# Optimization experiments

Measured on AMD Instinct MI355X. Metric: run time of the kernel, lower is better.

Reference implementation:

```python
import jax, jax.numpy as jnp
import numpy as np

EPS = 1e-6

def _l2norm(t):
    # F.normalize over channel axis (axis=1) of (B, dk, L)
    n = jnp.sqrt(jnp.sum(t * t, axis=1, keepdims=True))
    return t / jnp.maximum(n, EPS)

def setup_inputs() -> dict:
    key = jax.random.key(0)
    ks = jax.random.split(key, 8)
    B, Cin, Cenc, dk, dv, H, W = 2, 64, 96, 64, 64, 96, 96
    return {
        "x": jax.random.normal(ks[0], (B, Cin, H, W), dtype=jnp.float32),
        "x_enc": jax.random.normal(ks[1], (B, Cenc, H, W), dtype=jnp.float32),
        "Wq": jax.random.normal(ks[2], (dk, Cenc), dtype=jnp.float32) * 0.05,
        "bq": jax.random.normal(ks[3], (dk,), dtype=jnp.float32) * 0.05,
        "Wk": jax.random.normal(ks[4], (dk, Cenc), dtype=jnp.float32) * 0.05,
        "bk": jax.random.normal(ks[5], (dk,), dtype=jnp.float32) * 0.05,
        "Wv": jax.random.normal(ks[6], (dv, Cin), dtype=jnp.float32) * 0.05,
        "bv": jax.random.normal(ks[7], (dv,), dtype=jnp.float32) * 0.05,
    }

def reference(x, x_enc, Wq, bq, Wk, bk, Wv, bv):
    B, _, H, W = x.shape
    L = H * W
    # 1x1 conv projections == channel matmuls, then flatten spatial dims
    Q = (jnp.einsum('bchw,kc->bkhw', x_enc, Wq) + bq[None, :, None, None]).reshape(B, -1, L)
    K = (jnp.einsum('bchw,kc->bkhw', x_enc, Wk) + bk[None, :, None, None]).reshape(B, -1, L)
    V = (jnp.einsum('bchw,kc->bkhw', x, Wv) + bv[None, :, None, None]).reshape(B, -1, L)
    # per-position L2 normalization over the dk channel axis ('l2' mode)
    Q = _l2norm(Q)
    K = _l2norm(K)
    # A[b,i,j] = sum_q Q[b,q,i] * K[b,q,j], softmax over j
    A = jax.nn.softmax(jnp.einsum('bqi,bqj->bij', Q, K), axis=-1)  # (B, L, L)
    R = jnp.einsum('bij,bvj->bvi', A, V)  # (B, dv, L)
    return R.reshape(B, -1, H, W)
```

## Files before the change

### kernel.cpp

```cpp
#include <hip/hip_runtime.h>
#include <hip/hip_bf16.h>
#include <math.h>

#define NB   2
#define CIN  64
#define CENC 96
#define DK   64
#define DV   64
#define LL   9216
#define QBLK 256
#define KVBLK 64
#define NQT  (LL/QBLK)
#define LOG2E 1.44269504088896340736f

typedef __attribute__((ext_vector_type(8)))  short short8;
typedef __attribute__((ext_vector_type(16))) float f32x16;
typedef __attribute__((ext_vector_type(2)))  unsigned int uint2v;
typedef unsigned int uint;

__device__ inline void gload16(const void* g, void* l) {
    __builtin_amdgcn_global_load_lds(
        (const __attribute__((address_space(1))) unsigned int*)g,
        (__attribute__((address_space(3))) unsigned int*)l, 16, 0, 0);
}

__device__ inline unsigned short f2bf(float f) {
    union { float f; uint u; } v; v.f = f;
    uint r = (v.u + 0x7FFFu + ((v.u >> 16) & 1u)) >> 16;
    return (unsigned short)r;
}

__device__ inline float bf2f(uint u) {
    union { uint u; float f; } c; c.u = u << 16; return c.f;
}

__device__ inline uint cvtpk(float lo, float hi) {
    uint r;
    asm("v_cvt_pk_bf16_f32 %0, %1, %2" : "=v"(r) : "v"(lo), "v"(hi));
    return r;
}

__device__ inline void plswap(uint& a, uint& b) {
#if __has_builtin(__builtin_amdgcn_permlane32_swap)
    uint2v r = __builtin_amdgcn_permlane32_swap(a, b, false, false);
    a = r.x; b = r.y;
#else
    const int lane = threadIdx.x & 63;
    uint t = (lane < 32) ? b : a;
    t = __shfl_xor(t, 32, 64);
    uint an = (lane < 32) ? a : t;
    uint bn = (lane < 32) ? t : b;
    a = an; b = bn;
#endif
}

__global__ __launch_bounds__(256) void proj_kernel(
    const float* __restrict__ x, const float* __restrict__ x_enc,
    const float* __restrict__ Wq, const float* __restrict__ bq,
    const float* __restrict__ Wk, const float* __restrict__ bk,
    const float* __restrict__ Wv, const float* __restrict__ bv,
    unsigned short* __restrict__ Qb, unsigned short* __restrict__ Kb,
    unsigned short* __restrict__ Vt, int nqk)
{
    __shared__ float sh[2 * CENC * 64];
    const int tid = threadIdx.x;

    if ((int)blockIdx.x < nqk) {
        float* Wt0 = sh;
        float* Wt1 = sh + CENC * 64;
        for (int idx = tid; idx < DK * CENC; idx += 256) {
            int k = idx / CENC, c = idx - k * CENC;
            Wt0[c * 64 + (k ^ (c & 31))] = Wq[idx];
            Wt1[c * 64 + (k ^ (c & 31))] = Wk[idx];
        }
        __syncthreads();

        const int w    = __builtin_amdgcn_readfirstlane(tid >> 6);
        const int lane = tid & 63;
        const int gw   = blockIdx.x * 4 + w;
        const int p0g  = gw * 16;
        const int b    = p0g / LL;
        const int p0   = p0g - b * LL;

        float qa[16], ka[16];
        const float bqv = bq[lane], bkv = bk[lane];
#pragma unroll
        for (int p = 0; p < 16; ++p) { qa[p] = bqv; ka[p] = bkv; }

        const float* xp = x_enc + (size_t)b * CENC * LL + p0;
#pragma unroll 4
        for (int c = 0; c < CENC; ++c) {
            const float wq = Wt0[c * 64 + (lane ^ (c & 31))];
            const float wk = Wt1[c * 64 + (lane ^ (c & 31))];
            const float4* xc4 = (const float4*)(xp + (size_t)c * LL);
#pragma unroll
            for (int p4 = 0; p4 < 4; ++p4) {
                const float4 xv = xc4[p4];
                qa[4 * p4 + 0] = fmaf(wq, xv.x, qa[4 * p4 + 0]);
                qa[4 * p4 + 1] = fmaf(wq, xv.y, qa[4 * p4 + 1]);
                qa[4 * p4 + 2] = fmaf(wq, xv.z, qa[4 * p4 + 2]);
                qa[4 * p4 + 3] = fmaf(wq, xv.w, qa[4 * p4 + 3]);
                ka[4 * p4 + 0] = fmaf(wk, xv.x, ka[4 * p4 + 0]);
                ka[4 * p4 + 1] = fmaf(wk, xv.y, ka[4 * p4 + 1]);
                ka[4 * p4 + 2] = fmaf(wk, xv.z, ka[4 * p4 + 2]);
                ka[4 * p4 + 3] = fmaf(wk, xv.w, ka[4 * p4 + 3]);
            }
        }

        unsigned short* qrow = Qb + (size_t)(b * LL + p0) * 64 + lane;
        unsigned short* krow = Kb + (size_t)(b * LL + p0) * 64 + lane;
#pragma unroll
        for (int p = 0; p < 16; ++p) {
            float sq = qa[p] * qa[p];
            float sk = ka[p] * ka[p];
#pragma unroll
            for (int m = 1; m < 64; m <<= 1) {
                sq += __shfl_xor(sq, m, 64);
                sk += __shfl_xor(sk, m, 64);
            }
            qrow[(size_t)p * 64] = f2bf(qa[p] * (LOG2E / fmaxf(sqrtf(sq), 1e-6f)));
            krow[(size_t)p * 64] = f2bf(ka[p] * (1.f / fmaxf(sqrtf(sk), 1e-6f)));
        }
    } else {
        float* Wt = sh;
        unsigned short* Vsh = (unsigned short*)(sh + CIN * 64);
        for (int idx = tid; idx < DV * CIN; idx += 256) {
            int v = idx / CIN, c = idx - v * CIN;
            Wt[c * 64 + (v ^ (c & 31))] = Wv[idx];
        }
        __syncthreads();

        const int w    = __builtin_amdgcn_readfirstlane(tid >> 6);
        const int lane = tid & 63;
        const int l0g  = ((int)blockIdx.x - nqk) * 64;
        const int b    = l0g / LL;
        const int l0   = l0g - b * LL;
        const int p0   = w * 16;

        float va[16];
        const float bvv = bv[lane];
#pragma unroll
        for (int p = 0; p < 16; ++p) va[p] = bvv;

        const float* xp = x + (size_t)b * CIN * LL + l0 + p0;
#pragma unroll 4
        for (int c = 0; c < CIN; ++c) {
            const float wv = Wt[c * 64 + (lane ^ (c & 31))];
            const float4* xc4 = (const float4*)(xp + (size_t)c * LL);
#pragma unroll
            for (int p4 = 0; p4 < 4; ++p4) {
                const float4 xv = xc4[p4];
                va[4 * p4 + 0] = fmaf(wv, xv.x, va[4 * p4 + 0]);
                va[4 * p4 + 1] = fmaf(wv, xv.y, va[4 * p4 + 1]);
                va[4 * p4 + 2] = fmaf(wv, xv.z, va[4 * p4 + 2]);
                va[4 * p4 + 3] = fmaf(wv, xv.w, va[4 * p4 + 3]);
            }
        }
#pragma unroll
        for (int p = 0; p < 16; ++p) Vsh[(p0 + p) * 64 + lane] = f2bf(va[p]);
        __syncthreads();

        const int v = tid & 63, w2 = tid >> 6;
        uint pk[8];
#pragma unroll
        for (int j = 0; j < 8; ++j)
            pk[j] = (uint)Vsh[(w2 * 16 + 2 * j) * 64 + v] |
                    ((uint)Vsh[(w2 * 16 + 2 * j + 1) * 64 + v] << 16);
        uint4* dst = (uint4*)(Vt + (size_t)b * 64 * LL + (size_t)v * LL + l0 + w2 * 16);
        dst[0] = make_uint4(pk[0], pk[1], pk[2], pk[3]);
        dst[1] = make_uint4(pk[4], pk[5], pk[6], pk[7]);
    }
}

__global__ __launch_bounds__(256, 2) void flash_kernel(
    const unsigned short* __restrict__ Qb,
    const unsigned short* __restrict__ Kb,
    const unsigned short* __restrict__ Vt,
    float* __restrict__ Sp, unsigned short* __restrict__ Rp,
    int JS, int nt)
{
    __shared__ unsigned short Sh[16384];

    const int bid0  = blockIdx.x;
    const int chunk = gridDim.x >> 3;
    const int bid   = (bid0 & 7) * chunk + (bid0 >> 3);

    const int qt  = bid % NQT;
    const int js  = (bid / NQT) % JS;
    const int b   = bid / (NQT * JS);
    const int tid = threadIdx.x;
    const int w = tid >> 6, lane = tid & 63;
    const int ln = lane & 31, h = lane >> 5;
    const int i0w = qt * QBLK + w * 64;

    short8 qf[2][4];
#pragma unroll
    for (int ig = 0; ig < 2; ++ig)
#pragma unroll
        for (int kc = 0; kc < 4; ++kc)
            qf[ig][kc] = *(const short8*)(Qb + ((size_t)(b * LL + i0w + ig * 32 + ln)) * 64 + kc * 16 + h * 8);

    int aK[4];
#pragma unroll
    for (int kc = 0; kc < 4; ++kc)
        aK[kc] = ln * 128 + ((((kc << 1) + h) ^ (ln & 7)) << 4);

    const int o0 = w * 1024 + lane * 16;
    const int r0 = o0 >> 7;
    const int c0 = ((o0 >> 4) & 7) ^ (r0 & 7);

    const unsigned short* KbB = Kb + (size_t)b * LL * 64;
    const unsigned short* VtB = Vt + (size_t)b * 64 * LL;
    const int jbase = js * nt * KVBLK;

    f32x16 racc[2][2];
#pragma unroll
    for (int ig = 0; ig < 2; ++ig)
#pragma unroll
        for (int vg = 0; vg < 2; ++vg)
#pragma unroll
            for (int r = 0; r < 16; ++r) racc[ig][vg][r] = 0.f;
    float ssum[2] = {0.f, 0.f};

    gload16(KbB + (size_t)(jbase + r0) * 64 + c0 * 8, (char*)Sh + w * 1024);
    gload16(KbB + (size_t)(jbase + 32 + r0) * 64 + c0 * 8, (char*)Sh + 4096 + w * 1024);
    gload16(VtB + (size_t)r0 * LL + jbase + c0 * 8, (char*)Sh + 16384 + w * 1024);
    gload16(VtB + (size_t)(32 + r0) * LL + jbase + c0 * 8, (char*)Sh + 16384 + 4096 + w * 1024);

    const unsigned short* pK = KbB + (size_t)(jbase + KVBLK + r0) * 64 + c0 * 8;
    const unsigned short* pV = VtB + (size_t)r0 * LL + jbase + KVBLK + c0 * 8;

#define PREF(BUFOFF)                                                            \
    do {                                                                        \
        gload16(pK,                    (char*)Sh + (BUFOFF) + w * 1024);        \
        gload16(pK + 32 * 64,          (char*)Sh + (BUFOFF) + 4096 + w * 1024); \
        gload16(pV,                    (char*)Sh + 16384 + (BUFOFF) + w * 1024);\
        gload16(pV + (size_t)32 * LL,  (char*)Sh + 16384 + (BUFOFF) + 4096 + w * 1024); \
        pK += KVBLK * 64; pV += KVBLK;                                          \
    } while (0)

#define COMPUTE(BUFOFF)                                                         \
    do {                                                                        \
        _Pragma("unroll")                                                       \
        for (int jt = 0; jt < 2; ++jt) {                                        \
            f32x16 sacc[2];                                                     \
            _Pragma("unroll")                                                   \
            for (int ig = 0; ig < 2; ++ig)                                      \
                _Pragma("unroll")                                               \
                for (int r = 0; r < 16; ++r) sacc[ig][r] = 0.f;                 \
            __builtin_amdgcn_s_setprio(1);                                      \
            _Pragma("unroll")                                                   \
            for (int kc = 0; kc < 4; ++kc) {                                    \
                const short8 kf = *(const short8*)((const char*)Sh + (BUFOFF) + jt * 4096 + aK[kc]); \
                sacc[0] = __builtin_amdgcn_mfma_f32_32x32x16_bf16(kf, qf[0][kc], sacc[0], 0, 0, 0); \
                sacc[1] = __builtin_amdgcn_mfma_f32_32x32x16_bf16(kf, qf[1][kc], sacc[1], 0, 0, 0); \
            }                                                                   \
            __builtin_amdgcn_s_setprio(0);                                      \
            short8 pf[2][2];                                                    \
            _Pragma("unroll")                                                   \
            for (int ig = 0; ig < 2; ++ig) {                                    \
                _Pragma("unroll")                                               \
                for (int r = 0; r < 16; ++r) sacc[ig][r] = __builtin_amdgcn_exp2f(sacc[ig][r]); \
                float s0 = 0.f;                                                 \
                _Pragma("unroll")                                               \
                for (int r = 0; r < 16; r += 4)                                 \
                    s0 += (sacc[ig][r] + sacc[ig][r + 1]) + (sacc[ig][r + 2] + sacc[ig][r + 3]); \
                ssum[ig] += s0;                                                 \
                _Pragma("unroll")                                               \
                for (int c = 0; c < 2; ++c) {                                   \
                    uint a0 = cvtpk(sacc[ig][8 * c + 0], sacc[ig][8 * c + 1]);  \
                    uint b0 = cvtpk(sacc[ig][8 * c + 4], sacc[ig][8 * c + 5]);  \
                    uint a1 = cvtpk(sacc[ig][8 * c + 2], sacc[ig][8 * c + 3]);  \
                    uint b1 = cvtpk(sacc[ig][8 * c + 6], sacc[ig][8 * c + 7]);  \
                    plswap(a0, b0);                                             \
                    plswap(a1, b1);                                             \
                    union { uint u[4]; short8 s; } P;                           \
                    P.u[0] = a0; P.u[1] = a1; P.u[2] = b0; P.u[3] = b1;         \
                    pf[ig][c] = P.s;                                            \
                }                                                               \
            }                                                                   \
            __builtin_amdgcn_s_setprio(1);                                      \
            _Pragma("unroll")                                                   \
            for (int c = 0; c < 2; ++c) {                                       \
                const int kcv = 2 * jt + c;                                     \
                _Pragma("unroll")                                               \
                for (int vg = 0; vg < 2; ++vg) {                                \
                    const short8 vf = *(const short8*)((const char*)Sh + 16384 + (BUFOFF) + vg * 4096 + aK[kcv]); \
                    racc[0][vg] = __builtin_amdgcn_mfma_f32_32x32x16_bf16(pf[0][c], vf, racc[0][vg], 0, 0, 0); \
                    racc[1][vg] = __builtin_amdgcn_mfma_f32_32x32x16_bf16(pf[1][c], vf, racc[1][vg], 0, 0, 0); \
                }                                                               \
            }                                                                   \
            __builtin_amdgcn_s_setprio(0);                                      \
        }                                                                       \
    } while (0)

    int t = 0;
    for (; t + 2 <= nt; t += 2) {
        __syncthreads();
        PREF(8192);
        COMPUTE(0);
        __syncthreads();
        if (t + 2 < nt) PREF(0);
        COMPUTE(8192);
    }
    if (t < nt) {
        __syncthreads();
        COMPUTE(0);
    }
#undef PREF
#undef COMPUTE

#pragma unroll
    for (int ig = 0; ig < 2; ++ig) {
        float s = ssum[ig] + __shfl_xor(ssum[ig], 32, 64);
        if (h == 0) Sp[(size_t)(b * JS + js) * LL + i0w + ig * 32 + ln] = s;
    }
    const size_t rBase = (size_t)(b * JS + js) * 64;
#pragma unroll
    for (int ig = 0; ig < 2; ++ig)
#pragma unroll
        for (int vg = 0; vg < 2; ++vg) {
            unsigned short* dst = Rp + (rBase + vg * 32 + ln) * (size_t)LL + i0w + ig * 32 + 4 * h;
#pragma unroll
            for (int rr = 0; rr < 4; ++rr) {
                uint2v val;
                val.x = cvtpk(racc[ig][vg][4 * rr + 0], racc[ig][vg][4 * rr + 1]);
                val.y = cvtpk(racc[ig][vg][4 * rr + 2], racc[ig][vg][4 * rr + 3]);
                *(uint2v*)&dst[8 * rr] = val;
            }
        }
}

__global__ __launch_bounds__(256) void combine_kernel(
    const float* __restrict__ Sp, const unsigned short* __restrict__ Rp,
    float* __restrict__ out, int JS)
{
    size_t g8 = ((size_t)blockIdx.x * 256 + threadIdx.x) * 8;
    int l = (int)(g8 % LL);
    int v = (int)((g8 / LL) % 64);
    int b = (int)(g8 / ((size_t)64 * LL));
    float s[8], r[8];
#pragma unroll
    for (int k = 0; k < 8; ++k) { s[k] = 0.f; r[k] = 0.f; }
    for (int js = 0; js < JS; ++js) {
        const float4 sv0 = *(const float4*)&Sp[(size_t)(b * JS + js) * LL + l];
        const float4 sv1 = *(const float4*)&Sp[(size_t)(b * JS + js) * LL + l + 4];
        const uint4 rv = *(const uint4*)&Rp[((size_t)(b * JS + js) * 64 + v) * LL + l];
        s[0] += sv0.x; s[1] += sv0.y; s[2] += sv0.z; s[3] += sv0.w;
        s[4] += sv1.x; s[5] += sv1.y; s[6] += sv1.z; s[7] += sv1.w;
        r[0] += bf2f(rv.x & 0xffffu); r[1] += bf2f(rv.x >> 16);
        r[2] += bf2f(rv.y & 0xffffu); r[3] += bf2f(rv.y >> 16);
        r[4] += bf2f(rv.z & 0xffffu); r[5] += bf2f(rv.z >> 16);
        r[6] += bf2f(rv.w & 0xffffu); r[7] += bf2f(rv.w >> 16);
    }
    *(float4*)&out[g8]     = make_float4(r[0] / s[0], r[1] / s[1], r[2] / s[2], r[3] / s[3]);
    *(float4*)&out[g8 + 4] = make_float4(r[4] / s[4], r[5] / s[5], r[6] / s[6], r[7] / s[7]);
}

extern "C" void kernel_launch(void* const* d_in, const int* in_sizes, int n_in,
                              void* d_out, int out_size, void* d_ws, size_t ws_size,
                              hipStream_t stream) {
    (void)in_sizes; (void)n_in; (void)out_size;
    const float* x     = (const float*)d_in[0];
    const float* x_enc = (const float*)d_in[1];
    const float* Wq    = (const float*)d_in[2];
    const float* bq    = (const float*)d_in[3];
    const float* Wk    = (const float*)d_in[4];
    const float* bk    = (const float*)d_in[5];
    const float* Wv    = (const float*)d_in[6];
    const float* bv    = (const float*)d_in[7];
    float* out = (float*)d_out;
    char* ws = (char*)d_ws;

    const size_t nBF = (size_t)NB * LL * 64 * 2;
    unsigned short* Qb = (unsigned short*)ws;
    unsigned short* Kb = (unsigned short*)(ws + nBF);
    unsigned short* Vt = (unsigned short*)(ws + 2 * nBF);

    int JS = 8;
    {
        const int cand[3] = {16, 12, 8};
        for (int ci = 0; ci < 3; ++ci) {
            JS = cand[ci];
            size_t need = 3 * nBF + (size_t)NB * JS * LL * 4 + (size_t)NB * JS * 64 * LL * 2;
            if (need <= ws_size) break;
        }
    }
    float* Sp = (float*)(ws + 3 * nBF);
    unsigned short* Rp = (unsigned short*)(ws + 3 * nBF + (size_t)NB * JS * LL * 4);
    int nt = (LL / JS) / KVBLK;

    const int nqk = NB * LL / 64;
    proj_kernel   <<<2 * nqk, 256, 0, stream>>>(x, x_enc, Wq, bq, Wk, bk, Wv, bv, Qb, Kb, Vt, nqk);
    flash_kernel  <<<NB * JS * NQT, 256, 0, stream>>>(Qb, Kb, Vt, Sp, Rp, JS, nt);
    combine_kernel<<<(NB * 64 * LL) / 2048, 256, 0, stream>>>(Sp, Rp, out, JS);
}
```

Baseline: 98.49 us.

## Split flash query tile across 8 waves of 32 rows instead of 4 waves of 64

The flash kernel now launches 512 threads, and each of its 8 waves owns 32 query rows instead of 64. The K/V tile loads are spread over more threads, so each thread issues one K and one V global-to-LDS load per tile instead of two of each. This halves per-wave accumulator and Q-fragment registers and raises the wave count per CU, aiming for better latency hiding. In exchange, each K/V fragment read from LDS now feeds half as many MFMAs, which doubles LDS read traffic per unit of compute, and the larger blocks synchronise more waves at each barrier.

```diff
diff --git a/kernel.cpp b/kernel.cpp
--- a/kernel.cpp
+++ b/kernel.cpp
@@ -172,7 +172,7 @@
     }
 }
 
-__global__ __launch_bounds__(256, 2) void flash_kernel(
+__global__ __launch_bounds__(512, 4) void flash_kernel(
     const unsigned short* __restrict__ Qb,
     const unsigned short* __restrict__ Kb,
     const unsigned short* __restrict__ Vt,
@@ -191,51 +191,42 @@
     const int tid = threadIdx.x;
     const int w = tid >> 6, lane = tid & 63;
     const int ln = lane & 31, h = lane >> 5;
-    const int i0w = qt * QBLK + w * 64;
-
-    short8 qf[2][4];
-#pragma unroll
-    for (int ig = 0; ig < 2; ++ig)
-#pragma unroll
-        for (int kc = 0; kc < 4; ++kc)
-            qf[ig][kc] = *(const short8*)(Qb + ((size_t)(b * LL + i0w + ig * 32 + ln)) * 64 + kc * 16 + h * 8);
+    const int i0w = qt * QBLK + w * 32;
+
+    short8 qf[4];
+#pragma unroll
+    for (int kc = 0; kc < 4; ++kc)
+        qf[kc] = *(const short8*)(Qb + ((size_t)(b * LL + i0w + ln)) * 64 + kc * 16 + h * 8);
 
     int aK[4];
 #pragma unroll
     for (int kc = 0; kc < 4; ++kc)
         aK[kc] = ln * 128 + ((((kc << 1) + h) ^ (ln & 7)) << 4);
 
-    const int o0 = w * 1024 + lane * 16;
-    const int r0 = o0 >> 7;
-    const int c0 = ((o0 >> 4) & 7) ^ (r0 & 7);
+    const int r0 = tid >> 3;
+    const int c0 = (tid & 7) ^ (r0 & 7);
 
     const unsigned short* KbB = Kb + (size_t)b * LL * 64;
     const unsigned short* VtB = Vt + (size_t)b * 64 * LL;
     const int jbase = js * nt * KVBLK;
 
-    f32x16 racc[2][2];
-#pragma unroll
-    for (int ig = 0; ig < 2; ++ig)
-#pragma unroll
-        for (int vg = 0; vg < 2; ++vg)
-#pragma unroll
-            for (int r = 0; r < 16; ++r) racc[ig][vg][r] = 0.f;
-    float ssum[2] = {0.f, 0.f};
-
-    gload16(KbB + (size_t)(jbase + r0) * 64 + c0 * 8, (char*)Sh + w * 1024);
-    gload16(KbB + (size_t)(jbase + 32 + r0) * 64 + c0 * 8, (char*)Sh + 4096 + w * 1024);
-    gload16(VtB + (size_t)r0 * LL + jbase + c0 * 8, (char*)Sh + 16384 + w * 1024);
-    gload16(VtB + (size_t)(32 + r0) * LL + jbase + c0 * 8, (char*)Sh + 16384 + 4096 + w * 1024);
+    f32x16 racc[2];
+#pragma unroll
+    for (int vg = 0; vg < 2; ++vg)
+#pragma unroll
+        for (int r = 0; r < 16; ++r) racc[vg][r] = 0.f;
+    float ssum = 0.f;
+
+    gload16(KbB + (size_t)(jbase + r0) * 64 + c0 * 8, (char*)Sh + tid * 16);
+    gload16(VtB + (size_t)r0 * LL + jbase + c0 * 8, (char*)Sh + 16384 + tid * 16);
 
     const unsigned short* pK = KbB + (size_t)(jbase + KVBLK + r0) * 64 + c0 * 8;
     const unsigned short* pV = VtB + (size_t)r0 * LL + jbase + KVBLK + c0 * 8;
 
 #define PREF(BUFOFF)                                                            \
     do {                                                                        \
-        gload16(pK,                    (char*)Sh + (BUFOFF) + w * 1024);        \
-        gload16(pK + 32 * 64,          (char*)Sh + (BUFOFF) + 4096 + w * 1024); \
-        gload16(pV,                    (char*)Sh + 16384 + (BUFOFF) + w * 1024);\
-        gload16(pV + (size_t)32 * LL,  (char*)Sh + 16384 + (BUFOFF) + 4096 + w * 1024); \
+        gload16(pK, (char*)Sh + (BUFOFF) + tid * 16);                           \
+        gload16(pV, (char*)Sh + 16384 + (BUFOFF) + tid * 16);                   \
         pK += KVBLK * 64; pV += KVBLK;                                          \
     } while (0)
 
@@ -243,41 +234,35 @@
     do {                                                                        \
         _Pragma("unroll")                                                       \
         for (int jt = 0; jt < 2; ++jt) {                                        \
-            f32x16 sacc[2];                                                     \
-            _Pragma("unroll")                                                   \
-            for (int ig = 0; ig < 2; ++ig)                                      \
-                _Pragma("unroll")                                               \
-                for (int r = 0; r < 16; ++r) sacc[ig][r] = 0.f;                 \
+            f32x16 sacc;                                                        \
+            _Pragma("unroll")                                                   \
+            for (int r = 0; r < 16; ++r) sacc[r] = 0.f;                         \
             __builtin_amdgcn_s_setprio(1);                                      \
             _Pragma("unroll")                                                   \
             for (int kc = 0; kc < 4; ++kc) {                                    \
                 const short8 kf = *(const short8*)((const char*)Sh + (BUFOFF) + jt * 4096 + aK[kc]); \
-                sacc[0] = __builtin_amdgcn_mfma_f32_32x32x16_bf16(kf, qf[0][kc], sacc[0], 0, 0, 0); \
-                sacc[1] = __builtin_amdgcn_mfma_f32_32x32x16_bf16(kf, qf[1][kc], sacc[1], 0, 0, 0); \
+                sacc = __builtin_amdgcn_mfma_f32_32x32x16_bf16(kf, qf[kc], sacc, 0, 0, 0); \
             }                                                                   \
             __builtin_amdgcn_s_setprio(0);                                      \
-            short8 pf[2][2];                                                    \
-            _Pragma("unroll")                                                   \
-            for (int ig = 0; ig < 2; ++ig) {                                    \
-                _Pragma("unroll")                                               \
-                for (int r = 0; r < 16; ++r) sacc[ig][r] = __builtin_amdgcn_exp2f(sacc[ig][r]); \
-                float s0 = 0.f;                                                 \
-                _Pragma("unroll")                                               \
-                for (int r = 0; r < 16; r += 4)                                 \
-                    s0 += (sacc[ig][r] + sacc[ig][r + 1]) + (sacc[ig][r + 2] + sacc[ig][r + 3]); \
-                ssum[ig] += s0;                                                 \
-                _Pragma("unroll")                                               \
-                for (int c = 0; c < 2; ++c) {                                   \
-                    uint a0 = cvtpk(sacc[ig][8 * c + 0], sacc[ig][8 * c + 1]);  \
-                    uint b0 = cvtpk(sacc[ig][8 * c + 4], sacc[ig][8 * c + 5]);  \
-                    uint a1 = cvtpk(sacc[ig][8 * c + 2], sacc[ig][8 * c + 3]);  \
-                    uint b1 = cvtpk(sacc[ig][8 * c + 6], sacc[ig][8 * c + 7]);  \
-                    plswap(a0, b0);                                             \
-                    plswap(a1, b1);                                             \
-                    union { uint u[4]; short8 s; } P;                           \
-                    P.u[0] = a0; P.u[1] = a1; P.u[2] = b0; P.u[3] = b1;         \
-                    pf[ig][c] = P.s;                                            \
-                }                                                               \
+            _Pragma("unroll")                                                   \
+            for (int r = 0; r < 16; ++r) sacc[r] = __builtin_amdgcn_exp2f(sacc[r]); \
+            float s0 = 0.f;                                                     \
+            _Pragma("unroll")                                                   \
+            for (int r = 0; r < 16; r += 4)                                     \
+                s0 += (sacc[r] + sacc[r + 1]) + (sacc[r + 2] + sacc[r + 3]);    \
+            ssum += s0;                                                         \
+            short8 pf[2];                                                       \
+            _Pragma("unroll")                                                   \
+            for (int c = 0; c < 2; ++c) {                                       \
+                uint a0 = cvtpk(sacc[8 * c + 0], sacc[8 * c + 1]);              \
+                uint b0 = cvtpk(sacc[8 * c + 4], sacc[8 * c + 5]);              \
+                uint a1 = cvtpk(sacc[8 * c + 2], sacc[8 * c + 3]);              \
+                uint b1 = cvtpk(sacc[8 * c + 6], sacc[8 * c + 7]);              \
+                plswap(a0, b0);                                                 \
+                plswap(a1, b1);                                                 \
+                union { uint u[4]; short8 s; } P;                               \
+                P.u[0] = a0; P.u[1] = a1; P.u[2] = b0; P.u[3] = b1;             \
+                pf[c] = P.s;                                                    \
             }                                                                   \
             __builtin_amdgcn_s_setprio(1);                                      \
             _Pragma("unroll")                                                   \
@@ -286,8 +271,7 @@
                 _Pragma("unroll")                                               \
                 for (int vg = 0; vg < 2; ++vg) {                                \
                     const short8 vf = *(const short8*)((const char*)Sh + 16384 + (BUFOFF) + vg * 4096 + aK[kcv]); \
-                    racc[0][vg] = __builtin_amdgcn_mfma_f32_32x32x16_bf16(pf[0][c], vf, racc[0][vg], 0, 0, 0); \
-                    racc[1][vg] = __builtin_amdgcn_mfma_f32_32x32x16_bf16(pf[1][c], vf, racc[1][vg], 0, 0, 0); \
+                    racc[vg] = __builtin_amdgcn_mfma_f32_32x32x16_bf16(pf[c], vf, racc[vg], 0, 0, 0); \
                 }                                                               \
             }                                                                   \
             __builtin_amdgcn_s_setprio(0);                                      \
@@ -310,25 +294,22 @@
 #undef PREF
 #undef COMPUTE
 
-#pragma unroll
-    for (int ig = 0; ig < 2; ++ig) {
-        float s = ssum[ig] + __shfl_xor(ssum[ig], 32, 64);
-        if (h == 0) Sp[(size_t)(b * JS + js) * LL + i0w + ig * 32 + ln] = s;
+    {
+        float s = ssum + __shfl_xor(ssum, 32, 64);
+        if (h == 0) Sp[(size_t)(b * JS + js) * LL + i0w + ln] = s;
     }
     const size_t rBase = (size_t)(b * JS + js) * 64;
 #pragma unroll
-    for (int ig = 0; ig < 2; ++ig)
-#pragma unroll
-        for (int vg = 0; vg < 2; ++vg) {
-            unsigned short* dst = Rp + (rBase + vg * 32 + ln) * (size_t)LL + i0w + ig * 32 + 4 * h;
-#pragma unroll
-            for (int rr = 0; rr < 4; ++rr) {
-                uint2v val;
-                val.x = cvtpk(racc[ig][vg][4 * rr + 0], racc[ig][vg][4 * rr + 1]);
-                val.y = cvtpk(racc[ig][vg][4 * rr + 2], racc[ig][vg][4 * rr + 3]);
-                *(uint2v*)&dst[8 * rr] = val;
-            }
-        }
+    for (int vg = 0; vg < 2; ++vg) {
+        unsigned short* dst = Rp + (rBase + vg * 32 + ln) * (size_t)LL + i0w + 4 * h;
+#pragma unroll
+        for (int rr = 0; rr < 4; ++rr) {
+            uint2v val;
+            val.x = cvtpk(racc[vg][4 * rr + 0], racc[vg][4 * rr + 1]);
+            val.y = cvtpk(racc[vg][4 * rr + 2], racc[vg][4 * rr + 3]);
+            *(uint2v*)&dst[8 * rr] = val;
+        }
+    }
 }
 
 __global__ __launch_bounds__(256) void combine_kernel(
@@ -392,6 +373,6 @@
 
     const int nqk = NB * LL / 64;
     proj_kernel   <<<2 * nqk, 256, 0, stream>>>(x, x_enc, Wq, bq, Wk, bk, Wv, bv, Qb, Kb, Vt, nqk);
-    flash_kernel  <<<NB * JS * NQT, 256, 0, stream>>>(Qb, Kb, Vt, Sp, Rp, JS, nt);
+    flash_kernel  <<<NB * JS * NQT, 512, 0, stream>>>(Qb, Kb, Vt, Sp, Rp, JS, nt);
     combine_kernel<<<(NB * 64 * LL) / 2048, 256, 0, stream>>>(Sp, Rp, out, JS);
 }
```

Result: no change. 97.39 us (median of 2 runs) (-1.1%).
